# Kernel optimization log

Measured on AMD Instinct MI355X. Metric: run time of the kernel, lower is better.

Reference implementation:

```python
import jax, jax.numpy as jnp
import numpy as np

WINDOW_SIZE = 2
MAX_POW = 3


def setup_inputs() -> dict:
    return {"t": 8, "h": 32, "w": 32}


def reference(t, h, w):
    N = t * h * w
    grid = jnp.stack(
        jnp.meshgrid(jnp.arange(t), jnp.arange(h), jnp.arange(w), indexing="ij"),
        axis=-1,
    ).reshape(N, 3)
    # [N, N, 3] absolute coordinate differences
    abs_diff = jnp.abs(grid[:, None, :] - grid[None, :, :])

    # Local window: all three axis-diffs within window_size
    mask_local = jnp.all(abs_diff <= WINDOW_SIZE, axis=-1)

    # Dilated sparse: along exactly one axis, diff in {2^0,...,2^(max_pow-1)},
    # other two axes equal. Single pass instead of max_pow*3 OR'd NxN temporaries.
    offsets = 2 ** jnp.arange(MAX_POW)  # [1, 2, 4]
    is_pow = jnp.any(abs_diff[..., :, None] == offsets, axis=-1)  # [N, N, 3]
    is_zero = abs_diff == 0  # [N, N, 3]
    mask_sparse = (
        (is_pow[..., 0] & is_zero[..., 1] & is_zero[..., 2])
        | (is_pow[..., 1] & is_zero[..., 0] & is_zero[..., 2])
        | (is_pow[..., 2] & is_zero[..., 0] & is_zero[..., 1])
    )

    mask_combined = mask_local | mask_sparse
    neg_inf = jnp.finfo(jnp.float32).min
    return jnp.where(mask_combined, jnp.float32(0.0), neg_inf)
```

## Files before the change

### kernel.cpp

```cpp
#include <hip/hip_runtime.h>
#include <cmath>

#define NEG_MASKED (-3.3895313892515355e+38f)

typedef float v4f __attribute__((ext_vector_type(4)));

__device__ __forceinline__ bool keep_elem(int dt, int dh, int dw) {
  return ((dt <= 2) & (dh <= 2) & (dw <= 2))
       | ((dt == 4) & (dh == 0) & (dw == 0))
       | ((dh == 4) & (dt == 0) & (dw == 0))
       | ((dw == 4) & (dt == 0) & (dh == 0));
}

__global__ __launch_bounds__(256) void mask_kernel_p4(
    const int* __restrict__ tp, const int* __restrict__ hp, const int* __restrict__ wp,
    float* __restrict__ out, int N) {
  const int h = hp[0];
  const int w = wp[0];
  const int hw = h * w;

  const int i  = blockIdx.y;
  const int jb = blockIdx.x * 4096 + threadIdx.x * 4;
  float* const row = out + (size_t)i * (size_t)N;

  const int band = 4 * hw + 4 * w + 4;
  const v4f cmask = {NEG_MASKED, NEG_MASKED, NEG_MASKED, NEG_MASKED};

  if (((hw & (hw - 1)) == 0) & ((w & (w - 1)) == 0) & (hw != 0) & (w != 0)) {
    const int lhw = __builtin_ctz((unsigned)hw);
    const int lw  = __builtin_ctz((unsigned)w);
    const int hm  = (hw >> lw) - 1;
    const int wm  = w - 1;
    const int ti = i >> lhw;
    const int hi = (i >> lw) & hm;
    const int wi = i & wm;

#pragma unroll
    for (int p = 0; p < 4; ++p) {
      const int j0 = jb + p * 1024;
      if ((j0 + 3 < i - band) | (j0 > i + band)) {
        *(v4f*)(row + j0) = cmask;
      } else {
        v4f v;
#pragma unroll
        for (int e = 0; e < 4; ++e) {
          const int j  = j0 + e;
          const int dt = abs(ti - (j >> lhw));
          const int dh = abs(hi - ((j >> lw) & hm));
          const int dw = abs(wi - (j & wm));
          v[e] = keep_elem(dt, dh, dw) ? 0.0f : NEG_MASKED;
        }
        *(v4f*)(row + j0) = v;
      }
    }
  } else {
    const int ti = i / hw;
    const int ir = i - ti * hw;
    const int hi = ir / w;
    const int wi = ir - hi * w;
#pragma unroll
    for (int p = 0; p < 4; ++p) {
      const int j0 = jb + p * 1024;
      if ((j0 + 3 < i - band) | (j0 > i + band)) {
        *(v4f*)(row + j0) = cmask;
      } else {
        int ct = j0 / hw;
        int jr = j0 - ct * hw;
        int ch = jr / w;
        int cw = jr - ch * w;
        v4f v;
#pragma unroll
        for (int e = 0; e < 4; ++e) {
          const int dt = abs(ti - ct);
          const int dh = abs(hi - ch);
          const int dw = abs(wi - cw);
          v[e] = keep_elem(dt, dh, dw) ? 0.0f : NEG_MASKED;
          ++cw;
          if (cw == w) { cw = 0; ++ch; if (ch == h) { ch = 0; ++ct; } }
        }
        *(v4f*)(row + j0) = v;
      }
    }
  }
}

__global__ __launch_bounds__(256) void mask_kernel_v4(
    const int* __restrict__ tp, const int* __restrict__ hp, const int* __restrict__ wp,
    float* __restrict__ out, int N) {
  const int h = hp[0];
  const int w = wp[0];
  const int hw = h * w;
  const int i  = blockIdx.y;
  const int ti = i / hw;
  const int ir = i - ti * hw;
  const int hi = ir / w;
  const int wi = ir - hi * w;

  const int j0 = (blockIdx.x * 256 + threadIdx.x) * 4;
  if (j0 >= N) return;

  int ct = j0 / hw;
  int jr = j0 - ct * hw;
  int ch = jr / w;
  int cw = jr - ch * w;

  v4f v;
#pragma unroll
  for (int e = 0; e < 4; ++e) {
    const int dt = abs(ti - ct);
    const int dh = abs(hi - ch);
    const int dw = abs(wi - cw);
    v[e] = keep_elem(dt, dh, dw) ? 0.0f : NEG_MASKED;
    ++cw;
    if (cw == w) { cw = 0; ++ch; if (ch == h) { ch = 0; ++ct; } }
  }
  *(v4f*)(out + (size_t)i * (size_t)N + (size_t)j0) = v;
}

__global__ __launch_bounds__(256) void mask_kernel_s(
    const int* __restrict__ tp, const int* __restrict__ hp, const int* __restrict__ wp,
    float* __restrict__ out, int N) {
  const int h = hp[0];
  const int w = wp[0];
  const int hw = h * w;
  const long long total = (long long)N * (long long)N;
  const long long idx = (long long)blockIdx.x * 256ll + (long long)threadIdx.x;
  if (idx >= total) return;
  const int i = (int)(idx / N);
  const int j = (int)(idx - (long long)i * N);
  const int ti = i / hw, ir = i - ti * hw, hi = ir / w, wi = ir - hi * w;
  const int tj = j / hw, jr = j - tj * hw, hj = jr / w, wj = jr - hj * w;
  const int dt = abs(ti - tj), dh = abs(hi - hj), dw = abs(wi - wj);
  out[idx] = keep_elem(dt, dh, dw) ? 0.0f : NEG_MASKED;
}

extern "C" void kernel_launch(void* const* d_in, const int* in_sizes, int n_in,
                              void* d_out, int out_size, void* d_ws, size_t ws_size,
                              hipStream_t stream) {
  const int* tp = (const int*)d_in[0];
  const int* hp = (const int*)d_in[1];
  const int* wp = (const int*)d_in[2];
  float* out = (float*)d_out;

  const long long os = (long long)out_size;
  int N = (int)floor(sqrt((double)os));
  while ((long long)(N + 1) * (long long)(N + 1) <= os) ++N;
  while ((long long)N * (long long)N > os) --N;

  if ((N & 4095) == 0) {
    dim3 grid(N / 4096, N, 1);
    mask_kernel_p4<<<grid, 256, 0, stream>>>(tp, hp, wp, out, N);
  } else if ((N & 3) == 0) {
    const int vecs_per_row = N / 4;
    dim3 grid((vecs_per_row + 255) / 256, N, 1);
    mask_kernel_v4<<<grid, 256, 0, stream>>>(tp, hp, wp, out, N);
  } else {
    const long long total = (long long)N * (long long)N;
    const int blocks = (int)((total + 255) / 256);
    mask_kernel_s<<<blocks, 256, 0, stream>>>(tp, hp, wp, out, N);
  }
}
```

Baseline: 252.9 us.

## Fill rows with mask constant then scatter the sparse set of kept neighbours

Each block now owns one output row. It first writes the masked constant across the whole row, then, after a barrier, 131 threads compute the fixed neighbour offsets (the 5x5x5 window plus six ±4 axis offsets) and scatter zeros to the valid column positions. This removes the per-element distance test and the band check, leaving a pure streaming write plus a small scatter. The cost is a double write for the kept positions, less parallelism per row (one block per row), and an unvectorized scatter. The hardcoded offset set relies on WINDOW_SIZE=2 and MAX_POW=3, where offsets 1 and 2 already fall inside the window.

```diff
diff --git a/kernel.cpp b/kernel.cpp
--- a/kernel.cpp
+++ b/kernel.cpp
@@ -5,139 +5,62 @@
 
 typedef float v4f __attribute__((ext_vector_type(4)));
 
-__device__ __forceinline__ bool keep_elem(int dt, int dh, int dw) {
-  return ((dt <= 2) & (dh <= 2) & (dw <= 2))
-       | ((dt == 4) & (dh == 0) & (dw == 0))
-       | ((dh == 4) & (dt == 0) & (dw == 0))
-       | ((dw == 4) & (dt == 0) & (dh == 0));
-}
-
-__global__ __launch_bounds__(256) void mask_kernel_p4(
-    const int* __restrict__ tp, const int* __restrict__ hp, const int* __restrict__ wp,
+__global__ __launch_bounds__(256) void mask_rows(
+    const int* __restrict__ hp, const int* __restrict__ wp,
     float* __restrict__ out, int N) {
   const int h = hp[0];
   const int w = wp[0];
   const int hw = h * w;
 
-  const int i  = blockIdx.y;
-  const int jb = blockIdx.x * 4096 + threadIdx.x * 4;
-  float* const row = out + (size_t)i * (size_t)N;
+  const int i = blockIdx.x;
+  float* __restrict__ row = out + (size_t)i * (size_t)N;
 
-  const int band = 4 * hw + 4 * w + 4;
-  const v4f cmask = {NEG_MASKED, NEG_MASKED, NEG_MASKED, NEG_MASKED};
+  if ((N & 3) == 0) {
+    const v4f c = {NEG_MASKED, NEG_MASKED, NEG_MASKED, NEG_MASKED};
+    v4f* __restrict__ r4 = (v4f*)row;
+    const int n4 = N >> 2;
+    for (int k = threadIdx.x; k < n4; k += 256)
+      r4[k] = c;
+  } else {
+    for (int k = threadIdx.x; k < N; k += 256)
+      row[k] = NEG_MASKED;
+  }
 
-  if (((hw & (hw - 1)) == 0) & ((w & (w - 1)) == 0) & (hw != 0) & (w != 0)) {
-    const int lhw = __builtin_ctz((unsigned)hw);
-    const int lw  = __builtin_ctz((unsigned)w);
-    const int hm  = (hw >> lw) - 1;
-    const int wm  = w - 1;
-    const int ti = i >> lhw;
-    const int hi = (i >> lw) & hm;
-    const int wi = i & wm;
+  __syncthreads();
 
-#pragma unroll
-    for (int p = 0; p < 4; ++p) {
-      const int j0 = jb + p * 1024;
-      if ((j0 + 3 < i - band) | (j0 > i + band)) {
-        *(v4f*)(row + j0) = cmask;
-      } else {
-        v4f v;
-#pragma unroll
-        for (int e = 0; e < 4; ++e) {
-          const int j  = j0 + e;
-          const int dt = abs(ti - (j >> lhw));
-          const int dh = abs(hi - ((j >> lw) & hm));
-          const int dw = abs(wi - (j & wm));
-          v[e] = keep_elem(dt, dh, dw) ? 0.0f : NEG_MASKED;
-        }
-        *(v4f*)(row + j0) = v;
-      }
-    }
-  } else {
-    const int ti = i / hw;
-    const int ir = i - ti * hw;
-    const int hi = ir / w;
-    const int wi = ir - hi * w;
-#pragma unroll
-    for (int p = 0; p < 4; ++p) {
-      const int j0 = jb + p * 1024;
-      if ((j0 + 3 < i - band) | (j0 > i + band)) {
-        *(v4f*)(row + j0) = cmask;
-      } else {
-        int ct = j0 / hw;
-        int jr = j0 - ct * hw;
-        int ch = jr / w;
-        int cw = jr - ch * w;
-        v4f v;
-#pragma unroll
-        for (int e = 0; e < 4; ++e) {
-          const int dt = abs(ti - ct);
-          const int dh = abs(hi - ch);
-          const int dw = abs(wi - cw);
-          v[e] = keep_elem(dt, dh, dw) ? 0.0f : NEG_MASKED;
-          ++cw;
-          if (cw == w) { cw = 0; ++ch; if (ch == h) { ch = 0; ++ct; } }
-        }
-        *(v4f*)(row + j0) = v;
-      }
-    }
-  }
-}
+  const int k = threadIdx.x;
+  if (k >= 131) return;
 
-__global__ __launch_bounds__(256) void mask_kernel_v4(
-    const int* __restrict__ tp, const int* __restrict__ hp, const int* __restrict__ wp,
-    float* __restrict__ out, int N) {
-  const int h = hp[0];
-  const int w = wp[0];
-  const int hw = h * w;
-  const int i  = blockIdx.y;
   const int ti = i / hw;
   const int ir = i - ti * hw;
   const int hi = ir / w;
   const int wi = ir - hi * w;
 
-  const int j0 = (blockIdx.x * 256 + threadIdx.x) * 4;
-  if (j0 >= N) return;
+  int dt, dh, dw;
+  if (k < 125) {
+    dw = k % 5 - 2;
+    dh = (k / 5) % 5 - 2;
+    dt = k / 25 - 2;
+  } else {
+    const int e = k - 125;
+    const int s = (e & 1) ? 4 : -4;
+    dt = dh = dw = 0;
+    if (e < 2)      dt = s;
+    else if (e < 4) dh = s;
+    else            dw = s;
+  }
 
-  int ct = j0 / hw;
-  int jr = j0 - ct * hw;
-  int ch = jr / w;
-  int cw = jr - ch * w;
-
-  v4f v;
-#pragma unroll
-  for (int e = 0; e < 4; ++e) {
-    const int dt = abs(ti - ct);
-    const int dh = abs(hi - ch);
-    const int dw = abs(wi - cw);
-    v[e] = keep_elem(dt, dh, dw) ? 0.0f : NEG_MASKED;
-    ++cw;
-    if (cw == w) { cw = 0; ++ch; if (ch == h) { ch = 0; ++ct; } }
-  }
-  *(v4f*)(out + (size_t)i * (size_t)N + (size_t)j0) = v;
-}
-
-__global__ __launch_bounds__(256) void mask_kernel_s(
-    const int* __restrict__ tp, const int* __restrict__ hp, const int* __restrict__ wp,
-    float* __restrict__ out, int N) {
-  const int h = hp[0];
-  const int w = wp[0];
-  const int hw = h * w;
-  const long long total = (long long)N * (long long)N;
-  const long long idx = (long long)blockIdx.x * 256ll + (long long)threadIdx.x;
-  if (idx >= total) return;
-  const int i = (int)(idx / N);
-  const int j = (int)(idx - (long long)i * N);
-  const int ti = i / hw, ir = i - ti * hw, hi = ir / w, wi = ir - hi * w;
-  const int tj = j / hw, jr = j - tj * hw, hj = jr / w, wj = jr - hj * w;
-  const int dt = abs(ti - tj), dh = abs(hi - hj), dw = abs(wi - wj);
-  out[idx] = keep_elem(dt, dh, dw) ? 0.0f : NEG_MASKED;
+  const int hj = hi + dh;
+  const int wj = wi + dw;
+  const int j = i + dt * hw + dh * w + dw;
+  if (((unsigned)hj < (unsigned)h) & ((unsigned)wj < (unsigned)w) &
+      ((unsigned)j < (unsigned)N))
+    row[j] = 0.0f;
 }
 
 extern "C" void kernel_launch(void* const* d_in, const int* in_sizes, int n_in,
                               void* d_out, int out_size, void* d_ws, size_t ws_size,
                               hipStream_t stream) {
-  const int* tp = (const int*)d_in[0];
   const int* hp = (const int*)d_in[1];
   const int* wp = (const int*)d_in[2];
   float* out = (float*)d_out;
@@ -146,17 +69,7 @@
   int N = (int)floor(sqrt((double)os));
   while ((long long)(N + 1) * (long long)(N + 1) <= os) ++N;
   while ((long long)N * (long long)N > os) --N;
+  if (N < 1) N = 1;
 
-  if ((N & 4095) == 0) {
-    dim3 grid(N / 4096, N, 1);
-    mask_kernel_p4<<<grid, 256, 0, stream>>>(tp, hp, wp, out, N);
-  } else if ((N & 3) == 0) {
-    const int vecs_per_row = N / 4;
-    dim3 grid((vecs_per_row + 255) / 256, N, 1);
-    mask_kernel_v4<<<grid, 256, 0, stream>>>(tp, hp, wp, out, N);
-  } else {
-    const long long total = (long long)N * (long long)N;
-    const int blocks = (int)((total + 255) / 256);
-    mask_kernel_s<<<blocks, 256, 0, stream>>>(tp, hp, wp, out, N);
-  }
+  mask_rows<<<dim3(N), dim3(256), 0, stream>>>(hp, wp, out, N);
 }
```

After: 257.3 us. No clear change (+1.8%).
